# Kernel tuning notes

Measured on AMD Instinct MI355X. Metric: run time of the kernel, lower is better.

## Reference

```python
import jax, jax.numpy as jnp
import numpy as np

N_NODES = 50000
N_EDGES = 800000
D_NODE = 64
D_EDGE = 64


def setup_inputs() -> dict:
    key = jax.random.key(0)
    ks = jax.random.split(key, 8)
    s = lambda fan_in: 1.0 / np.sqrt(fan_in)
    return {
        "feats": jax.random.normal(ks[0], (N_NODES, D_NODE), dtype=jnp.float32),
        "edge_index": jax.random.randint(ks[1], (N_EDGES, 2), 0, N_NODES, dtype=jnp.int64),
        "edge_attr": jax.random.normal(ks[2], (N_EDGES, D_EDGE), dtype=jnp.float32),
        "W1e": jax.random.normal(ks[3], (2 * D_NODE + D_EDGE, 64), dtype=jnp.float32) * s(192),
        "b1e": jnp.zeros((64,), dtype=jnp.float32),
        "W2e": jax.random.normal(ks[4], (64, D_EDGE), dtype=jnp.float32) * s(64),
        "b2e": jnp.zeros((D_EDGE,), dtype=jnp.float32),
        "W1n": jax.random.normal(ks[5], (D_NODE + D_EDGE, 64), dtype=jnp.float32) * s(128),
        "b1n": jnp.zeros((64,), dtype=jnp.float32),
        "W2n": jax.random.normal(ks[6], (64, D_NODE), dtype=jnp.float32) * s(64),
        "b2n": jnp.zeros((D_NODE,), dtype=jnp.float32),
    }


def reference(feats, edge_index, edge_attr, W1e, b1e, W2e, b2e, W1n, b1n, W2n, b2n):
    r = edge_index[:, 0]
    c = edge_index[:, 1]
    n_nodes = feats.shape[0]

    # Edge model: gather source/target node feats, concat with edge_attr, MLP.
    x = jnp.concatenate([feats[r], feats[c], edge_attr], axis=1)  # [E, 2*d_node+d_edge]
    e = jax.nn.relu(x @ W1e + b1e) @ W2e + b2e                    # [E, d_edge]

    # Node model: mean-aggregate incoming edge messages by target node, concat, MLP.
    agg = jax.ops.segment_sum(e, c, num_segments=n_nodes)         # [N, d_edge]
    deg = jax.ops.segment_sum(jnp.ones((e.shape[0], 1), e.dtype), c, num_segments=n_nodes)
    agg = agg / jnp.maximum(deg, 1.0)
    h = jnp.concatenate([feats, agg], axis=1)                     # [N, d_node+d_edge]
    feats_out = jax.nn.relu(h @ W1n + b1n) @ W2n + b2n            # [N, d_node]

    return feats_out, e
```

## Files before the change

kernel.cpp:

```cpp
#include <hip/hip_runtime.h>

#define NN 50000
#define NE 800000
#define D 64

__device__ __forceinline__ void mlp_accum64(const float* __restrict__ x,
                                            const float* __restrict__ W,
                                            float scale, float* h) {
    const float4* x4 = (const float4*)x;
    #pragma unroll 1
    for (int k0 = 0; k0 < D; k0 += 8) {
        float xa[8];
        float4 v0 = x4[k0 / 4];
        float4 v1 = x4[k0 / 4 + 1];
        xa[0] = v0.x; xa[1] = v0.y; xa[2] = v0.z; xa[3] = v0.w;
        xa[4] = v1.x; xa[5] = v1.y; xa[6] = v1.z; xa[7] = v1.w;
        #pragma unroll
        for (int kk = 0; kk < 8; ++kk) {
            const float xk = xa[kk] * scale;
            const float* Wr = W + (k0 + kk) * D;
            #pragma unroll
            for (int j = 0; j < D; ++j) h[j] = fmaf(xk, Wr[j], h[j]);
        }
    }
}

__device__ __forceinline__ void mlp_layer2(const float* __restrict__ W2,
                                           const float* __restrict__ b2,
                                           const float* h, float* acc,
                                           float* myrow) {
    #pragma unroll
    for (int j = 0; j < D; ++j) acc[j] = b2[j];
    #pragma unroll
    for (int half = 0; half < 2; ++half) {
        #pragma unroll
        for (int k = 0; k < 32; ++k) myrow[k] = fmaxf(h[half * 32 + k], 0.f);
        #pragma unroll 1
        for (int k = 0; k < 32; ++k) {
            const float hk = myrow[k];
            const float* Wr = W2 + (half * 32 + k) * D;
            #pragma unroll
            for (int j = 0; j < D; ++j) acc[j] = fmaf(hk, Wr[j], acc[j]);
        }
    }
}

__global__ __launch_bounds__(256) void edge_kernel(
    const float* __restrict__ feats, const int* __restrict__ ei,
    const float* __restrict__ ea, const float* __restrict__ W1,
    const float* __restrict__ b1, const float* __restrict__ W2,
    const float* __restrict__ b2, float* __restrict__ e_out,
    float* __restrict__ agg, float* __restrict__ deg) {
    __shared__ float myrow_s[256 * 33];
    __shared__ float tbuf[4][64 * 17];
    __shared__ int cbuf[4][64];
    const int tid = threadIdx.x;
    const int w = tid >> 6;
    const int lane = tid & 63;
    const int eid = blockIdx.x * 256 + tid;
    const int ebase = blockIdx.x * 256 + w * 64;

    const int2 rc = ((const int2*)ei)[eid];
    const int r = rc.x;
    const int c = rc.y;

    float h[D];
    #pragma unroll
    for (int j = 0; j < D; ++j) h[j] = b1[j];

    const float* xr = feats + (size_t)r * D;
    const float* xc = feats + (size_t)c * D;
    const float* xe = ea + (size_t)eid * D;

    #pragma unroll 1
    for (int s = 0; s < 3; ++s) {
        const float* xp = (s == 0) ? xr : ((s == 1) ? xc : xe);
        mlp_accum64(xp, W1 + s * D * D, 1.0f, h);
    }

    float acc[D];
    mlp_layer2(W2, b2, h, acc, myrow_s + tid * 33);

    cbuf[w][lane] = c;
    float* T = tbuf[w];
    const int es = lane >> 4;
    const int js = lane & 15;
    #pragma unroll 1
    for (int c0 = 0; c0 < D; c0 += 16) {
        #pragma unroll
        for (int i = 0; i < 16; ++i) T[lane * 17 + i] = acc[c0 + i];
        #pragma unroll 1
        for (int g = 0; g < 16; ++g) {
            const int o = g * 4 + es;
            const float v = T[o * 17 + js];
            const int cd = cbuf[w][o];
            e_out[(size_t)(ebase + o) * D + c0 + js] = v;
            unsafeAtomicAdd(agg + (size_t)cd * D + c0 + js, v);
        }
    }
    unsafeAtomicAdd(deg + c, 1.0f);
}

__global__ __launch_bounds__(64) void node_kernel(
    const float* __restrict__ feats, const float* __restrict__ agg,
    const float* __restrict__ deg, const float* __restrict__ W1,
    const float* __restrict__ b1, const float* __restrict__ W2,
    const float* __restrict__ b2, float* __restrict__ out) {
    __shared__ float sh[64 * 33];
    const int tid = threadIdx.x;
    const int n = blockIdx.x * 64 + tid;
    if (n >= NN) return;

    float h[D];
    #pragma unroll
    for (int j = 0; j < D; ++j) h[j] = b1[j];

    const float rd = 1.0f / fmaxf(deg[n], 1.0f);

    mlp_accum64(feats + (size_t)n * D, W1, 1.0f, h);
    mlp_accum64(agg + (size_t)n * D, W1 + D * D, rd, h);

    float acc[D];
    mlp_layer2(W2, b2, h, acc, sh + tid * 33);

    float4* o4 = (float4*)(out + (size_t)n * D);
    #pragma unroll
    for (int q = 0; q < 16; ++q)
        o4[q] = make_float4(acc[4 * q + 0], acc[4 * q + 1],
                            acc[4 * q + 2], acc[4 * q + 3]);
}

extern "C" void kernel_launch(void* const* d_in, const int* in_sizes, int n_in,
                              void* d_out, int out_size, void* d_ws,
                              size_t ws_size, hipStream_t stream) {
    const float* feats = (const float*)d_in[0];
    const int* ei      = (const int*)d_in[1];
    const float* ea    = (const float*)d_in[2];
    const float* W1e   = (const float*)d_in[3];
    const float* b1e   = (const float*)d_in[4];
    const float* W2e   = (const float*)d_in[5];
    const float* b2e   = (const float*)d_in[6];
    const float* W1n   = (const float*)d_in[7];
    const float* b1n   = (const float*)d_in[8];
    const float* W2n   = (const float*)d_in[9];
    const float* b2n   = (const float*)d_in[10];

    float* out_f = (float*)d_out;
    float* feats_out = out_f;
    float* e_out = out_f + (size_t)NN * D;

    float* agg = (float*)d_ws;
    float* deg = agg + (size_t)NN * D;

    hipMemsetAsync(d_ws, 0, ((size_t)NN * D + NN) * sizeof(float), stream);

    edge_kernel<<<NE / 256, 256, 0, stream>>>(feats, ei, ea, W1e, b1e, W2e,
                                              b2e, e_out, agg, deg);
    node_kernel<<<(NN + 63) / 64, 64, 0, stream>>>(feats, agg, deg, W1n, b1n,
                                                   W2n, b2n, feats_out);
}
```

Baseline: 924.8 us.

## Compute edge layer-2 per output column into transpose buffer and add nontemporal I/O

The edge kernel no longer builds a full 64-float layer-2 accumulator array. It computes each output column as a dot product of the ReLU'd hidden vector with a W2 column, written straight into the shared transpose buffer. This removes the acc[64] registers and the 33KB myrow shared buffer, which should raise occupancy, at the cost of strided W2 column reads. Streaming edge_attr and edge_index loads and e_out stores now use nontemporal hints to reduce cache pollution.

```diff
diff --git a/kernel.cpp b/kernel.cpp
--- a/kernel.cpp
+++ b/kernel.cpp
@@ -4,17 +4,27 @@
 #define NE 800000
 #define D 64
 
+typedef float v4f __attribute__((ext_vector_type(4)));
+typedef int v2i __attribute__((ext_vector_type(2)));
+
+template <bool NT>
 __device__ __forceinline__ void mlp_accum64(const float* __restrict__ x,
                                             const float* __restrict__ W,
                                             float scale, float* h) {
-    const float4* x4 = (const float4*)x;
+    const v4f* x4 = (const v4f*)x;
     #pragma unroll 1
     for (int k0 = 0; k0 < D; k0 += 8) {
+        v4f v0, v1;
+        if (NT) {
+            v0 = __builtin_nontemporal_load(x4 + k0 / 4);
+            v1 = __builtin_nontemporal_load(x4 + k0 / 4 + 1);
+        } else {
+            v0 = x4[k0 / 4];
+            v1 = x4[k0 / 4 + 1];
+        }
         float xa[8];
-        float4 v0 = x4[k0 / 4];
-        float4 v1 = x4[k0 / 4 + 1];
-        xa[0] = v0.x; xa[1] = v0.y; xa[2] = v0.z; xa[3] = v0.w;
-        xa[4] = v1.x; xa[5] = v1.y; xa[6] = v1.z; xa[7] = v1.w;
+        xa[0] = v0[0]; xa[1] = v0[1]; xa[2] = v0[2]; xa[3] = v0[3];
+        xa[4] = v1[0]; xa[5] = v1[1]; xa[6] = v1[2]; xa[7] = v1[3];
         #pragma unroll
         for (int kk = 0; kk < 8; ++kk) {
             const float xk = xa[kk] * scale;
@@ -51,7 +61,6 @@
     const float* __restrict__ b1, const float* __restrict__ W2,
     const float* __restrict__ b2, float* __restrict__ e_out,
     float* __restrict__ agg, float* __restrict__ deg) {
-    __shared__ float myrow_s[256 * 33];
     __shared__ float tbuf[4][64 * 17];
     __shared__ int cbuf[4][64];
     const int tid = threadIdx.x;
@@ -60,9 +69,10 @@
     const int eid = blockIdx.x * 256 + tid;
     const int ebase = blockIdx.x * 256 + w * 64;
 
-    const int2 rc = ((const int2*)ei)[eid];
-    const int r = rc.x;
-    const int c = rc.y;
+    const v2i rc = __builtin_nontemporal_load((const v2i*)ei + eid);
+    const int r = rc[0];
+    const int c = rc[1];
+    cbuf[w][lane] = c;
 
     float h[D];
     #pragma unroll
@@ -73,28 +83,39 @@
     const float* xe = ea + (size_t)eid * D;
 
     #pragma unroll 1
-    for (int s = 0; s < 3; ++s) {
-        const float* xp = (s == 0) ? xr : ((s == 1) ? xc : xe);
-        mlp_accum64(xp, W1 + s * D * D, 1.0f, h);
-    }
+    for (int s = 0; s < 2; ++s)
+        mlp_accum64<false>((s == 0) ? xr : xc, W1 + s * D * D, 1.0f, h);
+    mlp_accum64<true>(xe, W1 + 2 * D * D, 1.0f, h);
 
-    float acc[D];
-    mlp_layer2(W2, b2, h, acc, myrow_s + tid * 33);
+    #pragma unroll
+    for (int k = 0; k < D; ++k) h[k] = fmaxf(h[k], 0.f);
 
-    cbuf[w][lane] = c;
     float* T = tbuf[w];
     const int es = lane >> 4;
     const int js = lane & 15;
     #pragma unroll 1
     for (int c0 = 0; c0 < D; c0 += 16) {
-        #pragma unroll
-        for (int i = 0; i < 16; ++i) T[lane * 17 + i] = acc[c0 + i];
+        #pragma unroll 1
+        for (int jj = 0; jj < 16; ++jj) {
+            const int j = c0 + jj;
+            const float* Wc = W2 + j;
+            float p0 = b2[j], p1 = 0.f, p2 = 0.f, p3 = 0.f;
+            #pragma unroll
+            for (int k = 0; k < D; k += 4) {
+                p0 = fmaf(h[k + 0], Wc[(k + 0) * D], p0);
+                p1 = fmaf(h[k + 1], Wc[(k + 1) * D], p1);
+                p2 = fmaf(h[k + 2], Wc[(k + 2) * D], p2);
+                p3 = fmaf(h[k + 3], Wc[(k + 3) * D], p3);
+            }
+            T[lane * 17 + jj] = (p0 + p1) + (p2 + p3);
+        }
         #pragma unroll 1
         for (int g = 0; g < 16; ++g) {
             const int o = g * 4 + es;
             const float v = T[o * 17 + js];
             const int cd = cbuf[w][o];
-            e_out[(size_t)(ebase + o) * D + c0 + js] = v;
+            __builtin_nontemporal_store(
+                v, e_out + (size_t)(ebase + o) * D + c0 + js);
             unsafeAtomicAdd(agg + (size_t)cd * D + c0 + js, v);
         }
     }
@@ -117,8 +138,8 @@
 
     const float rd = 1.0f / fmaxf(deg[n], 1.0f);
 
-    mlp_accum64(feats + (size_t)n * D, W1, 1.0f, h);
-    mlp_accum64(agg + (size_t)n * D, W1 + D * D, rd, h);
+    mlp_accum64<false>(feats + (size_t)n * D, W1, 1.0f, h);
+    mlp_accum64<false>(agg + (size_t)n * D, W1 + D * D, rd, h);
 
     float acc[D];
     mlp_layer2(W2, b2, h, acc, sh + tid * 33);
```

Result: faster. 855.6 us (-7.5%).
